# Kernel tuning notes

Hardware: AMD Instinct MI355X
Metric: run time of the kernel (lower is better)

## Reference

```python
import jax, jax.numpy as jnp
import numpy as np

B, L, H, E = 4, 2048, 16, 64
S, D = L, E

def setup_inputs() -> dict:
    key = jax.random.key(0)
    kq, kk, kv = jax.random.split(key, 3)
    queries = jax.random.normal(kq, (B, L, H, E), dtype=jnp.float32)
    keys = jax.random.normal(kk, (B, S, H, E), dtype=jnp.float32)
    values = jax.random.normal(kv, (B, S, H, D), dtype=jnp.float32)
    return {"queries": queries, "keys": keys, "values": values}

def reference(queries, keys, values):
    # FullAttention with mask_flag=True, attn_mask=None -> causal mask; dropout p=0 (eval).
    b, l, h, e = queries.shape
    scale = 1.0 / jnp.sqrt(jnp.asarray(e, queries.dtype))
    # scores: [B,H,L,S]
    scores = jnp.einsum('blhe,bshe->bhls', queries, keys)
    causal = jnp.triu(jnp.ones((l, l), dtype=bool), k=1)  # True above diagonal -> masked
    scores = jnp.where(causal[None, None, :, :], -jnp.inf, scores)
    A = jax.nn.softmax(scale * scores, axis=-1)
    V = jnp.einsum('bhls,bshd->blhd', A, values)
    return V
```

## Files before the change

### kernel.cpp

```cpp
#include <hip/hip_runtime.h>
#include <math.h>

#define BB 4
#define LL 2048
#define HH 16
#define EE 64
#define HE (HH*EE)

constexpr int QBLK  = 128;
constexpr int KVBLK = 64;
constexpr int NW    = 8;
constexpr int NQT   = LL / QBLK;
constexpr int NT    = LL / KVBLK;
constexpr int LDK   = 72;
constexpr float SCL2E = 0.18033688011112042f;
constexpr float DEFER_THR = 8.0f;

typedef short short8 __attribute__((ext_vector_type(8)));
typedef float f32x4  __attribute__((ext_vector_type(4)));

#define MFMA(a, b, c) __builtin_amdgcn_mfma_f32_16x16x32_bf16((a), (b), (c), 0, 0, 0)

#define GLD_LDS16(gp, lp)                                                     \
    __builtin_amdgcn_global_load_lds(                                         \
        (const __attribute__((address_space(1))) void*)(gp),                  \
        (__attribute__((address_space(3))) void*)(lp), 16, 0, 0)

static __device__ __forceinline__ unsigned short f2bf(float f) {
    unsigned u = __float_as_uint(f);
    return (unsigned short)((u + 0x7FFFu + ((u >> 16) & 1u)) >> 16);
}

__global__ __launch_bounds__(512, 2)
void prepass_cvt(const float* __restrict__ K, const float* __restrict__ V,
                 short* __restrict__ Kw, short* __restrict__ Vw)
{
    __shared__ short Vs[KVBLK][74];
    const int bid = blockIdx.x;
    const int bh  = bid >> 5, t = bid & 31;
    const int b   = bh >> 4, h = bh & 15;
    const int j0  = t * KVBLK;
    const int tid = threadIdx.x;
    const int row = tid >> 3;
    const int ch8 = (tid & 7) * 8;
    const size_t gbase = (size_t)b * LL * HE + (size_t)h * EE;
    const size_t obase = (size_t)bid * (64 * 64);

    {
        const float* kp = K + gbase + (size_t)(j0 + row) * HE + ch8;
        float4 a0 = *(const float4*)kp, a1 = *(const float4*)(kp + 4);
        float fv[8] = {a0.x,a0.y,a0.z,a0.w,a1.x,a1.y,a1.z,a1.w};
        short8 hv;
        #pragma unroll
        for (int i = 0; i < 8; ++i) hv[i] = (short)f2bf(fv[i]);
        *(short8*)(Kw + obase + row * 64 + (ch8 ^ ((row & 7) * 8))) = hv;
    }
    {
        const float* vp = V + gbase + (size_t)(j0 + row) * HE + ch8;
        float4 b0 = *(const float4*)vp, b1 = *(const float4*)(vp + 4);
        float gv[8] = {b0.x,b0.y,b0.z,b0.w,b1.x,b1.y,b1.z,b1.w};
        short8 vv;
        #pragma unroll
        for (int i = 0; i < 8; ++i) vv[i] = (short)f2bf(gv[i]);
        *(short8*)(&Vs[row][ch8]) = vv;
    }
    __syncthreads();
    {
        short8 ov;
        #pragma unroll
        for (int i = 0; i < 8; ++i) ov[i] = Vs[ch8 + i][row];
        *(short8*)(Vw + obase + row * 64 + (ch8 ^ ((row & 7) * 8))) = ov;
    }
}

__global__ __launch_bounds__(512, 4)
void attn_fast(const float* __restrict__ Q, const short* __restrict__ Kw,
               const short* __restrict__ Vw, float* __restrict__ O)
{
    __shared__ alignas(16) short Ks[KVBLK * 64];
    __shared__ alignas(16) short Vt[EE * 64];
    __shared__ short Pl[NW * 16 * LDK];

    const int bid = blockIdx.x;
    const int qt  = (NQT - 1) - (bid >> 6);
    const int bh  = bid & 63;
    const int b   = bh >> 4, h = bh & 15;
    const size_t base = (size_t)b * LL * HE + (size_t)h * EE;

    const int tid  = threadIdx.x;
    const int wave = tid >> 6, lane = tid & 63;
    const int g    = lane >> 4, c = lane & 15;
    const int swz  = (c & 7) * 8;

    const int q0 = qt * QBLK + wave * 16;
    const size_t kvbase = (size_t)bh * (NT * 64 * 64);

    short8 qf[2];
    {
        const float* qp = Q + base + (size_t)(q0 + c) * HE + 8 * g;
        #pragma unroll
        for (int ec = 0; ec < 2; ++ec) {
            float4 f0 = *(const float4*)(qp + ec * 32);
            float4 f1 = *(const float4*)(qp + ec * 32 + 4);
            float fv[8] = {f0.x, f0.y, f0.z, f0.w, f1.x, f1.y, f1.z, f1.w};
            #pragma unroll
            for (int i = 0; i < 8; ++i)
                qf[ec][i] = (short)f2bf(fv[i] * SCL2E);
        }
    }

    f32x4 o[4];
    #pragma unroll
    for (int db = 0; db < 4; ++db)
        #pragma unroll
        for (int j = 0; j < 4; ++j) o[db][j] = 0.0f;
    float m_r[4] = {-INFINITY, -INFINITY, -INFINITY, -INFINITY};
    float l_r[4] = {0.f, 0.f, 0.f, 0.f};

    const int ntile = 2 * qt + 2;

    for (int t = 0; t < ntile; ++t) {
        const int j0 = t * KVBLK;

        __syncthreads();
        {
            const size_t goff = kvbase + (size_t)t * 4096
                              + (size_t)(wave * 64 + lane) * 8;
            GLD_LDS16(Kw + goff, Ks + wave * 512);
            GLD_LDS16(Vw + goff, Vt + wave * 512);
        }
        __syncthreads();

        if (j0 <= q0 + 15) {
            const bool diag = (j0 + KVBLK - 1) > q0;

            f32x4 s[4];
            __builtin_amdgcn_s_setprio(1);
            #pragma unroll
            for (int kb = 0; kb < 4; ++kb) {
                f32x4 acc; acc[0]=0.f; acc[1]=0.f; acc[2]=0.f; acc[3]=0.f;
                const int roff = (kb * 16 + c) * 64;
                short8 k0 = *(const short8*)(&Ks[roff + ((8 * g) ^ swz)]);
                short8 k1 = *(const short8*)(&Ks[roff + ((32 + 8 * g) ^ swz)]);
                acc = MFMA(qf[0], k0, acc);
                acc = MFMA(qf[1], k1, acc);
                s[kb] = acc;
            }
            __builtin_amdgcn_s_setprio(0);

            float tm[4];
            #pragma unroll
            for (int r = 0; r < 4; ++r) {
                if (diag) {
                    const int qrow = q0 + 4 * g + r;
                    #pragma unroll
                    for (int kb = 0; kb < 4; ++kb)
                        if (j0 + kb * 16 + c > qrow) s[kb][r] = -INFINITY;
                }
                tm[r] = fmaxf(fmaxf(s[0][r], s[1][r]), fmaxf(s[2][r], s[3][r]));
                #pragma unroll
                for (int xm = 1; xm <= 8; xm <<= 1)
                    tm[r] = fmaxf(tm[r], __shfl_xor(tm[r], xm));
            }

            #pragma unroll
            for (int r = 0; r < 4; ++r) {
                const float nm = fmaxf(m_r[r], tm[r]);
                if (nm - m_r[r] > DEFER_THR) {
                    const float corr = __builtin_amdgcn_exp2f(m_r[r] - nm);
                    l_r[r] *= corr;
                    #pragma unroll
                    for (int db = 0; db < 4; ++db) o[db][r] *= corr;
                    m_r[r] = nm;
                }
                #pragma unroll
                for (int kb = 0; kb < 4; ++kb) {
                    const float p = __builtin_amdgcn_exp2f(s[kb][r] - m_r[r]);
                    l_r[r] += p;
                    Pl[(wave * 16 + 4 * g + r) * LDK + kb * 16 + c] = (short)f2bf(p);
                }
            }

            #pragma unroll
            for (int kc = 0; kc < 2; ++kc) {
                short8 pa = *(const short8*)(&Pl[(wave * 16 + c) * LDK + kc * 32 + 8 * g]);
                __builtin_amdgcn_s_setprio(1);
                #pragma unroll
                for (int db = 0; db < 4; ++db) {
                    const int voff = (db * 16 + c) * 64 + ((kc * 32 + 8 * g) ^ swz);
                    short8 vb = *(const short8*)(&Vt[voff]);
                    o[db] = MFMA(pa, vb, o[db]);
                }
                __builtin_amdgcn_s_setprio(0);
            }
        }
    }

    #pragma unroll
    for (int r = 0; r < 4; ++r) {
        float ls = l_r[r];
        #pragma unroll
        for (int xm = 1; xm <= 8; xm <<= 1) ls += __shfl_xor(ls, xm);
        const float inv = 1.0f / ls;
        float* op = O + base + (size_t)(q0 + 4 * g + r) * HE + c;
        #pragma unroll
        for (int db = 0; db < 4; ++db)
            op[db * 16] = o[db][r] * inv;
    }
}

__global__ __launch_bounds__(512, 4)
void attn_mfma(const float* __restrict__ Q, const float* __restrict__ K,
               const float* __restrict__ V, float* __restrict__ O)
{
    __shared__ short Ks[KVBLK * LDK];
    __shared__ short Vt[EE * LDK];
    __shared__ short Pl[NW * 16 * LDK];

    const int bid = blockIdx.x;
    const int qt  = (NQT - 1) - (bid >> 6);
    const int bh  = bid & 63;
    const int b   = bh >> 4, h = bh & 15;
    const size_t base = (size_t)b * LL * HE + (size_t)h * EE;

    const int tid  = threadIdx.x;
    const int wave = tid >> 6, lane = tid & 63;
    const int g    = lane >> 4, c = lane & 15;

    const int q0 = qt * QBLK + wave * 16;

    short8 qf[2];
    {
        const float* qp = Q + base + (size_t)(q0 + c) * HE + 8 * g;
        #pragma unroll
        for (int ec = 0; ec < 2; ++ec) {
            float4 f0 = *(const float4*)(qp + ec * 32);
            float4 f1 = *(const float4*)(qp + ec * 32 + 4);
            float fv[8] = {f0.x, f0.y, f0.z, f0.w, f1.x, f1.y, f1.z, f1.w};
            #pragma unroll
            for (int i = 0; i < 8; ++i)
                qf[ec][i] = (short)f2bf(fv[i] * SCL2E);
        }
    }

    f32x4 o[4];
    #pragma unroll
    for (int db = 0; db < 4; ++db)
        #pragma unroll
        for (int j = 0; j < 4; ++j) o[db][j] = 0.0f;
    float m_r[4] = {-INFINITY, -INFINITY, -INFINITY, -INFINITY};
    float l_r[4] = {0.f, 0.f, 0.f, 0.f};

    const int ntile = 2 * qt + 2;
    const int srow = tid >> 3;
    const int scc  = (tid & 7) * 8;

    for (int t = 0; t < ntile; ++t) {
        const int j0 = t * KVBLK;

        __syncthreads();
        {
            const float* kp = K + base + (size_t)(j0 + srow) * HE + scc;
            float4 a0 = *(const float4*)(kp);
            float4 a1 = *(const float4*)(kp + 4);
            float fv[8] = {a0.x, a0.y, a0.z, a0.w, a1.x, a1.y, a1.z, a1.w};
            short8 hv;
            #pragma unroll
            for (int i = 0; i < 8; ++i) hv[i] = (short)f2bf(fv[i]);
            *(short8*)(&Ks[srow * LDK + scc]) = hv;

            const float* vp = V + base + (size_t)(j0 + srow) * HE + scc;
            float4 b0 = *(const float4*)(vp);
            float4 b1 = *(const float4*)(vp + 4);
            float gv[8] = {b0.x, b0.y, b0.z, b0.w, b1.x, b1.y, b1.z, b1.w};
            #pragma unroll
            for (int i = 0; i < 8; ++i) {
                const int d = scc + i;
                const int col = srow ^ (((d >> 3) & 7) << 3);
                Vt[d * LDK + col] = (short)f2bf(gv[i]);
            }
        }
        __syncthreads();

        if (j0 <= q0 + 15) {
            const bool diag = (j0 + KVBLK - 1) > q0;

            f32x4 s[4];
            __builtin_amdgcn_s_setprio(1);
            #pragma unroll
            for (int kb = 0; kb < 4; ++kb) {
                f32x4 acc; acc[0]=0.f; acc[1]=0.f; acc[2]=0.f; acc[3]=0.f;
                const int roff = (kb * 16 + c) * LDK + 8 * g;
                short8 k0 = *(const short8*)(&Ks[roff]);
                short8 k1 = *(const short8*)(&Ks[roff + 32]);
                acc = MFMA(qf[0], k0, acc);
                acc = MFMA(qf[1], k1, acc);
                s[kb] = acc;
            }
            __builtin_amdgcn_s_setprio(0);

            float tm[4];
            #pragma unroll
            for (int r = 0; r < 4; ++r) {
                if (diag) {
                    const int qrow = q0 + 4 * g + r;
                    #pragma unroll
                    for (int kb = 0; kb < 4; ++kb)
                        if (j0 + kb * 16 + c > qrow) s[kb][r] = -INFINITY;
                }
                tm[r] = fmaxf(fmaxf(s[0][r], s[1][r]), fmaxf(s[2][r], s[3][r]));
                #pragma unroll
                for (int xm = 1; xm <= 8; xm <<= 1)
                    tm[r] = fmaxf(tm[r], __shfl_xor(tm[r], xm));
            }

            #pragma unroll
            for (int r = 0; r < 4; ++r) {
                const float nm = fmaxf(m_r[r], tm[r]);
                if (nm - m_r[r] > DEFER_THR) {
                    const float corr = __builtin_amdgcn_exp2f(m_r[r] - nm);
                    l_r[r] *= corr;
                    #pragma unroll
                    for (int db = 0; db < 4; ++db) o[db][r] *= corr;
                    m_r[r] = nm;
                }
                #pragma unroll
                for (int kb = 0; kb < 4; ++kb) {
                    const float p = __builtin_amdgcn_exp2f(s[kb][r] - m_r[r]);
                    l_r[r] += p;
                    Pl[(wave * 16 + 4 * g + r) * LDK + kb * 16 + c] = (short)f2bf(p);
                }
            }

            #pragma unroll
            for (int kc = 0; kc < 2; ++kc) {
                short8 pa = *(const short8*)(&Pl[(wave * 16 + c) * LDK + kc * 32 + 8 * g]);
                __builtin_amdgcn_s_setprio(1);
                #pragma unroll
                for (int db = 0; db < 4; ++db) {
                    const int d  = db * 16 + c;
                    const int k0 = (kc * 32 + 8 * g) ^ (((d >> 3) & 7) << 3);
                    short8 vb = *(const short8*)(&Vt[d * LDK + k0]);
                    o[db] = MFMA(pa, vb, o[db]);
                }
                __builtin_amdgcn_s_setprio(0);
            }
        }
    }

    #pragma unroll
    for (int r = 0; r < 4; ++r) {
        float ls = l_r[r];
        #pragma unroll
        for (int xm = 1; xm <= 8; xm <<= 1) ls += __shfl_xor(ls, xm);
        const float inv = 1.0f / ls;
        float* op = O + base + (size_t)(q0 + 4 * g + r) * HE + c;
        #pragma unroll
        for (int db = 0; db < 4; ++db)
            op[db * 16] = o[db][r] * inv;
    }
}

extern "C" void kernel_launch(void* const* d_in, const int* in_sizes, int n_in,
                              void* d_out, int out_size, void* d_ws, size_t ws_size,
                              hipStream_t stream) {
    const float* Q = (const float*)d_in[0];
    const float* K = (const float*)d_in[1];
    const float* V = (const float*)d_in[2];
    float* Out = (float*)d_out;

    const size_t kv_shorts = (size_t)64 * NT * 64 * 64;
    const size_t need = 2 * kv_shorts * sizeof(short);

    if (ws_size >= need) {
        short* Kw = (short*)d_ws;
        short* Vw = Kw + kv_shorts;
        hipLaunchKernelGGL(prepass_cvt, dim3(64 * NT), dim3(512), 0, stream, K, V, Kw, Vw);
        hipLaunchKernelGGL(attn_fast, dim3(BB * HH * NQT), dim3(512), 0, stream, Q, Kw, Vw, Out);
    } else {
        hipLaunchKernelGGL(attn_mfma, dim3(BB * HH * NQT), dim3(512), 0, stream, Q, K, V, Out);
    }
}
```

Measured before the change: 213.0 us.

## Double-buffer K/V tiles in LDS and pack bf16 conversion of probabilities

```diff
diff --git a/kernel.cpp b/kernel.cpp
--- a/kernel.cpp
+++ b/kernel.cpp
@@ -29,6 +29,12 @@
 static __device__ __forceinline__ unsigned short f2bf(float f) {
     unsigned u = __float_as_uint(f);
     return (unsigned short)((u + 0x7FFFu + ((u >> 16) & 1u)) >> 16);
+}
+
+static __device__ __forceinline__ unsigned cvt_pk_bf16(float lo, float hi) {
+    unsigned r;
+    asm("v_cvt_pk_bf16_f32 %0, %1, %2" : "=v"(r) : "v"(lo), "v"(hi));
+    return r;
 }
 
 __global__ __launch_bounds__(512, 2)
@@ -77,8 +83,8 @@
 void attn_fast(const float* __restrict__ Q, const short* __restrict__ Kw,
                const short* __restrict__ Vw, float* __restrict__ O)
 {
-    __shared__ alignas(16) short Ks[KVBLK * 64];
-    __shared__ alignas(16) short Vt[EE * 64];
+    __shared__ alignas(16) short Ks[2][KVBLK * 64];
+    __shared__ alignas(16) short Vt[2][EE * 64];
     __shared__ short Pl[NW * 16 * LDK];
 
     const int bid = blockIdx.x;
@@ -94,6 +100,7 @@
 
     const int q0 = qt * QBLK + wave * 16;
     const size_t kvbase = (size_t)bh * (NT * 64 * 64);
+    const size_t lane8  = (size_t)(wave * 64 + lane) * 8;
 
     short8 qf[2];
     {
@@ -119,20 +126,25 @@
 
     const int ntile = 2 * qt + 2;
 
+    GLD_LDS16(Kw + kvbase + lane8, &Ks[0][wave * 512]);
+    GLD_LDS16(Vw + kvbase + lane8, &Vt[0][wave * 512]);
+
+    int cur = 0;
     for (int t = 0; t < ntile; ++t) {
         const int j0 = t * KVBLK;
 
         __syncthreads();
-        {
-            const size_t goff = kvbase + (size_t)t * 4096
-                              + (size_t)(wave * 64 + lane) * 8;
-            GLD_LDS16(Kw + goff, Ks + wave * 512);
-            GLD_LDS16(Vw + goff, Vt + wave * 512);
-        }
-        __syncthreads();
+
+        if (t + 1 < ntile) {
+            const size_t goff = kvbase + (size_t)(t + 1) * 4096 + lane8;
+            GLD_LDS16(Kw + goff, &Ks[cur ^ 1][wave * 512]);
+            GLD_LDS16(Vw + goff, &Vt[cur ^ 1][wave * 512]);
+        }
 
         if (j0 <= q0 + 15) {
             const bool diag = (j0 + KVBLK - 1) > q0;
+            const short* ksb = &Ks[cur][0];
+            const short* vtb = &Vt[cur][0];
 
             f32x4 s[4];
             __builtin_amdgcn_s_setprio(1);
@@ -140,8 +152,8 @@
             for (int kb = 0; kb < 4; ++kb) {
                 f32x4 acc; acc[0]=0.f; acc[1]=0.f; acc[2]=0.f; acc[3]=0.f;
                 const int roff = (kb * 16 + c) * 64;
-                short8 k0 = *(const short8*)(&Ks[roff + ((8 * g) ^ swz)]);
-                short8 k1 = *(const short8*)(&Ks[roff + ((32 + 8 * g) ^ swz)]);
+                short8 k0 = *(const short8*)(&ksb[roff + ((8 * g) ^ swz)]);
+                short8 k1 = *(const short8*)(&ksb[roff + ((32 + 8 * g) ^ swz)]);
                 acc = MFMA(qf[0], k0, acc);
                 acc = MFMA(qf[1], k1, acc);
                 s[kb] = acc;
@@ -157,7 +169,7 @@
                     for (int kb = 0; kb < 4; ++kb)
                         if (j0 + kb * 16 + c > qrow) s[kb][r] = -INFINITY;
                 }
-                tm[r] = fmaxf(fmaxf(s[0][r], s[1][r]), fmaxf(s[2][r], s[3][r]));
+                tm[r] = fmaxf(fmaxf(fmaxf(s[0][r], s[1][r]), s[2][r]), s[3][r]);
                 #pragma unroll
                 for (int xm = 1; xm <= 8; xm <<= 1)
                     tm[r] = fmaxf(tm[r], __shfl_xor(tm[r], xm));
@@ -173,12 +185,18 @@
                     for (int db = 0; db < 4; ++db) o[db][r] *= corr;
                     m_r[r] = nm;
                 }
-                #pragma unroll
-                for (int kb = 0; kb < 4; ++kb) {
-                    const float p = __builtin_amdgcn_exp2f(s[kb][r] - m_r[r]);
-                    l_r[r] += p;
-                    Pl[(wave * 16 + 4 * g + r) * LDK + kb * 16 + c] = (short)f2bf(p);
-                }
+                const float p0 = __builtin_amdgcn_exp2f(s[0][r] - m_r[r]);
+                const float p1 = __builtin_amdgcn_exp2f(s[1][r] - m_r[r]);
+                const float p2 = __builtin_amdgcn_exp2f(s[2][r] - m_r[r]);
+                const float p3 = __builtin_amdgcn_exp2f(s[3][r] - m_r[r]);
+                l_r[r] += (p0 + p1) + (p2 + p3);
+                const unsigned pk01 = cvt_pk_bf16(p0, p1);
+                const unsigned pk23 = cvt_pk_bf16(p2, p3);
+                short* prow = &Pl[(wave * 16 + 4 * g + r) * LDK + c];
+                prow[0]  = (short)pk01;
+                prow[16] = (short)(pk01 >> 16);
+                prow[32] = (short)pk23;
+                prow[48] = (short)(pk23 >> 16);
             }
 
             #pragma unroll
@@ -188,12 +206,13 @@
                 #pragma unroll
                 for (int db = 0; db < 4; ++db) {
                     const int voff = (db * 16 + c) * 64 + ((kc * 32 + 8 * g) ^ swz);
-                    short8 vb = *(const short8*)(&Vt[voff]);
+                    short8 vb = *(const short8*)(&vtb[voff]);
                     o[db] = MFMA(pa, vb, o[db]);
                 }
                 __builtin_amdgcn_s_setprio(0);
             }
         }
+        cur ^= 1;
     }
 
     #pragma unroll
```

New measurement: 211.0 us. Within noise of the previous version (-1.0%).
